# Kernel tuning notes

Measured on AMD Instinct MI355X. Metric: run time of the kernel, lower is better.

Reference implementation:

```python
import jax, jax.numpy as jnp
from jax import lax
import numpy as np
import math

B, T, HID = 4, 2048, 1024
NH, KS, INTER = 8, 4, 2816
HD = HID // NH
CHUNK = 32
EPS = 1e-6


def setup_inputs() -> dict:
    key = jax.random.key(0)
    ks = jax.random.split(key, 16)
    def w(k, shape, fan_in):
        return jax.random.normal(k, shape, jnp.float32) * (1.0 / math.sqrt(fan_in))
    logit = math.log(0.95 / 0.05)
    return {
        'x': jax.random.normal(ks[0], (B, T, HID), jnp.float32),
        'qkv_w': w(ks[1], (3 * HID, HID), HID),
        'out_proj_w': w(ks[2], (HID, HID), HID),
        'out_gate_w': w(ks[3], (HID, HID), HID),
        'out_gate_b': jnp.zeros((HID,), jnp.float32),
        'decay_param': jnp.full((NH,), logit, jnp.float32),
        'conv_w': w(ks[4], (HID, 1, KS), KS),      # depthwise: [out, in/groups=1, k]
        'conv_b': jnp.zeros((HID,), jnp.float32),
        'pw_w': w(ks[5], (HID, HID), HID),
        'gate_w': w(ks[6], (HID, 2 * HID), 2 * HID),
        'w1': w(ks[7], (INTER, HID), HID),
        'w2': w(ks[8], (INTER, HID), HID),
        'w3': w(ks[9], (HID, INTER), INTER),
        'norm1_w': jnp.ones((HID,), jnp.float32),
        'norm2_w': jnp.ones((HID,), jnp.float32),
    }


def rmsnorm(x, w, eps=EPS):
    ms = jnp.mean(jnp.square(x), axis=-1, keepdims=True)
    return x * lax.rsqrt(ms + eps) * w


def decay_scan(x, decay, init):
    # inclusive scan out[t] = decay*out[t-1] + x[t]; x:[B,NH,T,HD], decay:[1,NH,1], init:[B,NH,HD]
    b, h, t, d = x.shape
    c = min(CHUNK, t)
    log_d = jnp.log(jnp.maximum(decay.astype(jnp.float32), 1e-8))        # [1,NH,1]
    idx = jnp.arange(c, dtype=jnp.float32)
    log_p = log_d[..., None] * idx[None, None, :, None]                  # [1,NH,c,1]
    p, inv_p = jnp.exp(log_p), jnp.exp(-log_p)
    init_p = jnp.exp(log_d[..., None] * (idx + 1.0)[None, None, :, None])
    xc = x.astype(jnp.float32).reshape(b, h, t // c, c, d)
    xc = jnp.moveaxis(xc, 2, 0)                                          # [Nc,B,NH,c,HD]
    def step(state, chunk):
        cs = jnp.cumsum(chunk * inv_p, axis=2)
        out = cs * p + state[:, :, None, :] * init_p
        return out[:, :, -1, :], out
    _, outs = lax.scan(step, init.astype(jnp.float32), xc)
    out = jnp.moveaxis(outs, 0, 2).reshape(b, h, t, d)
    return out.astype(x.dtype)


def _forward(x, qkv_w, out_proj_w, out_gate_w, out_gate_b, decay_param,
             conv_w, conv_b, pw_w, gate_w, w1, w2, w3, norm1_w, norm2_w):
    b, t, _ = x.shape
    h = rmsnorm(x, norm1_w)

    # ---- LocalConv (depthwise causal conv + pointwise) ----
    xc = jnp.transpose(h, (0, 2, 1))                                     # [B,HID,T]
    pad = jnp.zeros((b, HID, KS - 1), x.dtype)
    xc = jnp.concatenate([pad, xc], axis=2)
    conv = lax.conv_general_dilated(xc, conv_w, (1,), 'VALID',
                                    dimension_numbers=('NCH', 'OIH', 'NCH'),
                                    feature_group_count=HID)
    conv = conv + conv_b[None, :, None]
    conv = jnp.transpose(conv, (0, 2, 1))                                # [B,T,HID]
    local = jnp.einsum('bth,oh->bto', jax.nn.silu(conv), pw_w)

    # ---- LinearAttention ----
    qkv = jnp.einsum('bth,oh->bto', h, qkv_w)
    q, k, v = jnp.split(qkv, 3, axis=-1)
    def heads(z):
        return jnp.transpose(z.reshape(b, t, NH, HD), (0, 2, 1, 3))      # [B,NH,T,HD]
    q, k, v = heads(q), heads(k), heads(v)
    q = jax.nn.elu(q) + 1.0
    k = jax.nn.elu(k) + 1.0
    decay = jax.nn.sigmoid(decay_param).reshape(1, NH, 1)
    zero_state = jnp.zeros((b, NH, HD), x.dtype)
    running_kv = decay_scan(k * v, decay, zero_state)
    running_ks = decay_scan(k, decay, zero_state)
    den = jnp.maximum(jnp.sum(q * running_ks, axis=-1, keepdims=True), 1e-6)
    o = q * running_kv / den                                             # [B,NH,T,HD]
    v_direct = jnp.transpose(v, (0, 2, 1, 3)).reshape(b, t, HID)
    o = jnp.transpose(o, (0, 2, 1, 3)).reshape(b, t, HID)
    g = jax.nn.sigmoid(jnp.einsum('bth,oh->bto', o, out_gate_w) + out_gate_b)
    o = g * o + (1.0 - g) * v_direct
    attn = jnp.einsum('bth,oh->bto', o, out_proj_w)

    # ---- Gate fusion of local/global, residual ----
    comb = jnp.concatenate([local, attn], axis=-1)
    gmix = jax.nn.sigmoid(jnp.einsum('bth,oh->bto', comb, gate_w))
    x = x + gmix * local + (1.0 - gmix) * attn

    # ---- FFN (SwiGLU) + residual ----
    h2 = rmsnorm(x, norm2_w)
    ffn = jnp.einsum('bti,oi->bto',
                     jax.nn.silu(jnp.einsum('bth,ih->bti', h2, w1)) *
                     jnp.einsum('bth,ih->bti', h2, w2), w3)
    return x + ffn


def reference(x, qkv_w, out_proj_w, out_gate_w, out_gate_b, decay_param,
              conv_w, conv_b, pw_w, gate_w, w1, w2, w3, norm1_w, norm2_w):
    return _forward(x, qkv_w, out_proj_w, out_gate_w, out_gate_b, decay_param,
                    conv_w, conv_b, pw_w, gate_w, w1, w2, w3, norm1_w, norm2_w)
```

## Files before the change

### kernel.cpp

```cpp
#include <hip/hip_runtime.h>
#include <math.h>

static constexpr int Bc    = 4;
static constexpr int Tc    = 2048;
static constexpr int HIDc  = 1024;
static constexpr int NHc   = 8;
static constexpr int HDc   = 128;
static constexpr int Mrows = Bc * Tc;
static constexpr int INTERc= 2816;
static constexpr int CH    = 64;
static constexpr int NC    = Tc / CH;

typedef _Float16 f16;
typedef __attribute__((ext_vector_type(8))) _Float16 f16x8;
typedef __attribute__((ext_vector_type(4))) float f32x4;
typedef unsigned short u16;

union H8 { f16 h[8]; int4 v; u16 u[8]; };
union H4 { f16 h[4]; int2 v; u16 u[4]; };
union F4 { float4 v; float a[4]; };

static __device__ __forceinline__ float sigm(float x) { return 1.0f / (1.0f + expf(-x)); }
static __device__ __forceinline__ float silu(float x) { return x * sigm(x); }
static __device__ __forceinline__ float elu1(float x) { return x > 0.0f ? x + 1.0f : expf(x); }

static __device__ __forceinline__ float h2f(u16 u){ f16 h; __builtin_memcpy(&h,&u,2); return (float)h; }
static __device__ __forceinline__ u16 f2h(float x){ f16 h=(f16)x; u16 u; __builtin_memcpy(&u,&h,2); return u; }
static __device__ __forceinline__ float rec2(u16 h, u16 l){ return h2f(h) + h2f(l); }
static __device__ __forceinline__ void fsplit(float v, u16& h, u16& l){ h = f2h(v); l = f2h(v - h2f(h)); }

static __device__ __forceinline__ void gld16(const u16* g, u16* l)
{
    __builtin_amdgcn_global_load_lds((const __attribute__((address_space(1))) void*)g,
                                     (__attribute__((address_space(3))) void*)l,
                                     16, 0, 0);
}

__global__ __launch_bounds__(256) void wcvt_k(const float* __restrict__ src,
                                              u16* __restrict__ dst, int n8)
{
    const int i = blockIdx.x * 256 + threadIdx.x;
    if (i >= n8) return;
    F4 a, b; a.v = ((const float4*)src)[i * 2]; b.v = ((const float4*)src)[i * 2 + 1];
    H8 o;
    #pragma unroll
    for (int u = 0; u < 4; u++) { o.h[u] = (f16)a.a[u]; o.h[4 + u] = (f16)b.a[u]; }
    ((int4*)dst)[i] = o.v;
}

template<int INPAIR>
__global__ __launch_bounds__(256) void rmsnorm_k(const float* __restrict__ xf,
                                                 const u16* __restrict__ xhi,
                                                 const u16* __restrict__ xlo,
                                                 const float* __restrict__ w,
                                                 u16* __restrict__ ohi,
                                                 u16* __restrict__ olo)
{
    const int row = blockIdx.x;
    const int tid = threadIdx.x;
    const size_t off = (size_t)row * HIDc + tid * 4;
    float xv[4];
    if constexpr (INPAIR) {
        H4 H, L;
        H.v = *(const int2*)(xhi + off);
        L.v = *(const int2*)(xlo + off);
        #pragma unroll
        for (int u = 0; u < 4; u++) xv[u] = (float)H.h[u] + (float)L.h[u];
    } else {
        F4 f; f.v = *(const float4*)(xf + off);
        #pragma unroll
        for (int u = 0; u < 4; u++) xv[u] = f.a[u];
    }
    float ss = xv[0]*xv[0] + xv[1]*xv[1] + xv[2]*xv[2] + xv[3]*xv[3];
    #pragma unroll
    for (int o = 32; o > 0; o >>= 1) ss += __shfl_xor(ss, o);
    __shared__ float sred[4];
    if ((tid & 63) == 0) sred[tid >> 6] = ss;
    __syncthreads();
    const float tot = sred[0] + sred[1] + sred[2] + sred[3];
    const float scale = rsqrtf(tot * (1.0f / (float)HIDc) + 1e-6f);
    F4 wv; wv.v = *(const float4*)(w + tid * 4);
    H4 OH, OL;
    #pragma unroll
    for (int u = 0; u < 4; u++) {
        u16 hh, ll; fsplit(xv[u] * scale * wv.a[u], hh, ll);
        OH.u[u] = hh; OL.u[u] = ll;
    }
    *(int2*)(ohi + off) = OH.v;
    *(int2*)(olo + off) = OL.v;
}

__global__ __launch_bounds__(256) void conv_k(const u16* __restrict__ hhi,
                                              const u16* __restrict__ hlo,
                                              const float* __restrict__ cw,
                                              const float* __restrict__ cb,
                                              u16* __restrict__ ohi,
                                              u16* __restrict__ olo)
{
    const int row = blockIdx.x;
    const int t   = row & (Tc - 1);
    const int ch4 = threadIdx.x * 4;
    const float* wp = cw + (size_t)ch4 * 4;
    F4 bias; bias.v = *(const float4*)(cb + ch4);
    F4 acc;
    #pragma unroll
    for (int u = 0; u < 4; u++) acc.a[u] = bias.a[u];
    #pragma unroll
    for (int j = 0; j < 4; j++) {
        const int tt = t - 3 + j;
        if (tt >= 0) {
            const size_t off = ((size_t)row + j - 3) * HIDc + ch4;
            H4 H, L;
            H.v = *(const int2*)(hhi + off);
            L.v = *(const int2*)(hlo + off);
            #pragma unroll
            for (int u = 0; u < 4; u++) acc.a[u] += ((float)H.h[u] + (float)L.h[u]) * wp[u * 4 + j];
        }
    }
    H4 OH, OL;
    #pragma unroll
    for (int u = 0; u < 4; u++) {
        u16 hh, ll; fsplit(silu(acc.a[u]), hh, ll);
        OH.u[u] = hh; OL.u[u] = ll;
    }
    const size_t off = (size_t)row * HIDc + ch4;
    *(int2*)(ohi + off) = OH.v;
    *(int2*)(olo + off) = OL.v;
}

__global__ __launch_bounds__(64) void scan1_k(u16* __restrict__ khi, u16* __restrict__ klo,
                                              const u16* __restrict__ vhi, const u16* __restrict__ vlo,
                                              u16* __restrict__ shi, u16* __restrict__ slo,
                                              const float* __restrict__ dp)
{
    const int bid = blockIdx.x;
    const int c   = bid & (NC - 1);
    const int bh  = bid >> 5;
    const int b   = bh >> 3, hh = bh & 7;
    const int lane = threadIdx.x;
    const float dec = sigm(dp[hh]);
    const size_t base = (size_t)b * Tc * HIDc + (size_t)(c * CH) * HIDc + hh * HDc + lane * 2;
    float skv0 = 0.f, skv1 = 0.f, sks0 = 0.f, sks1 = 0.f;
    for (int t = 0; t < CH; t++) {
        const size_t p = base + (size_t)t * HIDc;
        const unsigned kh = *(const unsigned*)(khi + p);
        const unsigned kl = *(const unsigned*)(klo + p);
        const unsigned vh = *(const unsigned*)(vhi + p);
        const unsigned vl = *(const unsigned*)(vlo + p);
        const float kx = elu1(rec2((u16)kh, (u16)kl));
        const float ky = elu1(rec2((u16)(kh >> 16), (u16)(kl >> 16)));
        const float vx = rec2((u16)vh, (u16)vl);
        const float vy = rec2((u16)(vh >> 16), (u16)(vl >> 16));
        skv0 = dec * skv0 + kx * vx;
        skv1 = dec * skv1 + ky * vy;
        sks0 = dec * sks0 + kx;
        sks1 = dec * sks1 + ky;
        u16 h0, l0, h1, l1;
        fsplit(skv0, h0, l0); fsplit(skv1, h1, l1);
        *(unsigned*)(khi + p) = (unsigned)h0 | ((unsigned)h1 << 16);
        *(unsigned*)(klo + p) = (unsigned)l0 | ((unsigned)l1 << 16);
        fsplit(sks0, h0, l0); fsplit(sks1, h1, l1);
        *(unsigned*)(shi + p) = (unsigned)h0 | ((unsigned)h1 << 16);
        *(unsigned*)(slo + p) = (unsigned)l0 | ((unsigned)l1 << 16);
    }
}

__global__ __launch_bounds__(64) void scan2_k(u16* __restrict__ qhi, u16* __restrict__ qlo,
                                              const u16* __restrict__ skvhi, const u16* __restrict__ skvlo,
                                              const u16* __restrict__ skshi, const u16* __restrict__ skslo,
                                              const float* __restrict__ dp)
{
    const int bid = blockIdx.x;
    const int c   = bid & (NC - 1);
    const int bh  = bid >> 5;
    const int b   = bh >> 3, hh = bh & 7;
    const int lane = threadIdx.x;
    const float dec = sigm(dp[hh]);
    float dCH = dec;
    #pragma unroll
    for (int i = 0; i < 6; i++) dCH *= dCH;
    const size_t rowbase = (size_t)b * Tc * HIDc + hh * HDc + lane * 2;

    float ckv0 = 0.f, ckv1 = 0.f, cks0 = 0.f, cks1 = 0.f;
    for (int j = 0; j < c; j++) {
        const size_t p = rowbase + (size_t)(j * CH + CH - 1) * HIDc;
        const unsigned ah = *(const unsigned*)(skvhi + p);
        const unsigned al = *(const unsigned*)(skvlo + p);
        const unsigned bh2 = *(const unsigned*)(skshi + p);
        const unsigned bl2 = *(const unsigned*)(skslo + p);
        ckv0 = ckv0 * dCH + rec2((u16)ah, (u16)al);
        ckv1 = ckv1 * dCH + rec2((u16)(ah >> 16), (u16)(al >> 16));
        cks0 = cks0 * dCH + rec2((u16)bh2, (u16)bl2);
        cks1 = cks1 * dCH + rec2((u16)(bh2 >> 16), (u16)(bl2 >> 16));
    }

    const size_t cbase = rowbase + (size_t)(c * CH) * HIDc;
    float pw = dec;
    for (int t = 0; t < CH; t++) {
        const size_t p = cbase + (size_t)t * HIDc;
        const unsigned qh = *(const unsigned*)(qhi + p);
        const unsigned ql = *(const unsigned*)(qlo + p);
        const unsigned ah = *(const unsigned*)(skvhi + p);
        const unsigned al = *(const unsigned*)(skvlo + p);
        const unsigned bh2 = *(const unsigned*)(skshi + p);
        const unsigned bl2 = *(const unsigned*)(skslo + p);
        const float qx = elu1(rec2((u16)qh, (u16)ql));
        const float qy = elu1(rec2((u16)(qh >> 16), (u16)(ql >> 16)));
        const float skv0 = rec2((u16)ah, (u16)al) + pw * ckv0;
        const float skv1 = rec2((u16)(ah >> 16), (u16)(al >> 16)) + pw * ckv1;
        const float sks0 = rec2((u16)bh2, (u16)bl2) + pw * cks0;
        const float sks1 = rec2((u16)(bh2 >> 16), (u16)(bl2 >> 16)) + pw * cks1;
        float part = qx * sks0 + qy * sks1;
        #pragma unroll
        for (int o = 32; o > 0; o >>= 1) part += __shfl_xor(part, o);
        const float inv = 1.0f / fmaxf(part, 1e-6f);
        u16 h0, l0, h1, l1;
        fsplit(qx * skv0 * inv, h0, l0);
        fsplit(qy * skv1 * inv, h1, l1);
        *(unsigned*)(qhi + p) = (unsigned)h0 | ((unsigned)h1 << 16);
        *(unsigned*)(qlo + p) = (unsigned)l0 | ((unsigned)l1 << 16);
        pw *= dec;
    }
}

template<int MODE, int PRE>
__global__ __launch_bounds__(256) void gemm_f16_k(
    const u16* __restrict__ Ahi, const u16* __restrict__ Alo,
    const u16* __restrict__ A2hi, const u16* __restrict__ A2lo, int lda,
    const u16* __restrict__ Wh, const float* __restrict__ Wf,
    float* __restrict__ Cout,
    u16* __restrict__ Chi, u16* __restrict__ Clo, int ldc,
    int K, int kSplit, int nx,
    const float* __restrict__ bias,
    const float* __restrict__ E0f,
    const u16* __restrict__ E0hi, const u16* __restrict__ E0lo, int ldE0,
    const u16* __restrict__ E1hi, const u16* __restrict__ E1lo, int ldE1,
    const u16* __restrict__ E2hi, const u16* __restrict__ E2lo, int ldE2)
{
    __shared__ __align__(16) u16 Ah[4][128][8];
    __shared__ __align__(16) u16 Al[4][128][8];
    __shared__ __align__(16) u16 Bs[4][128][8];

    const int tid  = threadIdx.x;
    const int lane = tid & 63;
    const int wv   = tid >> 6;
    const int wr   = wv >> 1, wc = wv & 1;
    const int lr   = lane & 15, lk = lane >> 4;

    const int cpx = gridDim.x >> 3;
    int bid = blockIdx.x;
    bid = (bid & 7) * cpx + (bid >> 3);
    const int n0 = (bid % nx) * 128;
    const int m0 = (bid / nx) * 128;

    f32x4 acc[4][4];
    #pragma unroll
    for (int i = 0; i < 4; i++)
        #pragma unroll
        for (int j = 0; j < 4; j++)
            acc[i][j] = (f32x4){0.f, 0.f, 0.f, 0.f};

    for (int k0 = 0; k0 < K; k0 += 32) {
        const u16* ah = Ahi; const u16* al = Alo; int kb = k0;
        if constexpr (MODE == 4) {
            if (k0 >= kSplit) { ah = A2hi; al = A2lo; kb = k0 - kSplit; }
        }
        const size_t a0off = (size_t)(m0 + lane) * lda + kb + wv * 8;
        const size_t a1off = a0off + (size_t)64 * lda;
        F4 wreg[4];
        size_t w0off = 0, w1off = 0;
        if constexpr (PRE) {
            w0off = (size_t)(n0 + lane) * K + k0 + wv * 8;
            w1off = w0off + (size_t)64 * K;
        } else {
            const float* wp0 = Wf + (size_t)(n0 + lane) * K + k0 + wv * 8;
            const float* wp1 = wp0 + (size_t)64 * K;
            wreg[0].v = *(const float4*)(wp0);
            wreg[1].v = *(const float4*)(wp0 + 4);
            wreg[2].v = *(const float4*)(wp1);
            wreg[3].v = *(const float4*)(wp1 + 4);
        }
        __syncthreads();
        gld16(ah + a0off, &Ah[wv][0][0]);
        gld16(ah + a1off, &Ah[wv][64][0]);
        gld16(al + a0off, &Al[wv][0][0]);
        gld16(al + a1off, &Al[wv][64][0]);
        if constexpr (PRE) {
            gld16(Wh + w0off, &Bs[wv][0][0]);
            gld16(Wh + w1off, &Bs[wv][64][0]);
        } else {
            H8 W0, W1;
            #pragma unroll
            for (int e = 0; e < 8; e++) {
                W0.h[e] = (f16)wreg[e >> 2].a[e & 3];
                W1.h[e] = (f16)wreg[2 + (e >> 2)].a[e & 3];
            }
            *(int4*)&Bs[wv][lane][0]      = W0.v;
            *(int4*)&Bs[wv][64 + lane][0] = W1.v;
        }
        __syncthreads();
        f16x8 av[4], au[4], bv[4];
        #pragma unroll
        for (int fi = 0; fi < 4; fi++) {
            av[fi] = *(const f16x8*)&Ah[lk][wr * 64 + fi * 16 + lr][0];
            au[fi] = *(const f16x8*)&Al[lk][wr * 64 + fi * 16 + lr][0];
            bv[fi] = *(const f16x8*)&Bs[lk][wc * 64 + fi * 16 + lr][0];
        }
        #pragma unroll
        for (int i = 0; i < 4; i++)
            #pragma unroll
            for (int j = 0; j < 4; j++) {
                acc[i][j] = __builtin_amdgcn_mfma_f32_16x16x32_f16(av[i], bv[j], acc[i][j], 0, 0, 0);
                acc[i][j] = __builtin_amdgcn_mfma_f32_16x16x32_f16(au[i], bv[j], acc[i][j], 0, 0, 0);
            }
    }

    #pragma unroll
    for (int i = 0; i < 4; i++) {
        #pragma unroll
        for (int j = 0; j < 4; j++) {
            #pragma unroll
            for (int v = 0; v < 4; v++) {
                const size_t r = (size_t)(m0 + wr * 64 + i * 16 + lk * 4 + v);
                const int c = n0 + wc * 64 + j * 16 + lr;
                const size_t idx = r * (size_t)ldc + c;
                float val = acc[i][j][v];
                if constexpr (MODE == 1) {
                    val = silu(val);
                } else if constexpr (MODE == 2) {
                    val = rec2(Chi[idx], Clo[idx]) * val;
                } else if constexpr (MODE == 3) {
                    const float g = sigm(val + bias[c]);
                    const size_t i0 = r * (size_t)ldE0 + c, i1 = r * (size_t)ldE1 + c;
                    val = g * rec2(E0hi[i0], E0lo[i0]) + (1.0f - g) * rec2(E1hi[i1], E1lo[i1]);
                } else if constexpr (MODE == 4) {
                    const float g = sigm(val);
                    const size_t i1 = r * (size_t)ldE1 + c, i2 = r * (size_t)ldE2 + c;
                    val = E0f[r * (size_t)ldE0 + c] + g * rec2(E1hi[i1], E1lo[i1])
                          + (1.0f - g) * rec2(E2hi[i2], E2lo[i2]);
                } else if constexpr (MODE == 6) {
                    Cout[idx] = rec2(Chi[idx], Clo[idx]) + val;
                    continue;
                }
                u16 hh, ll; fsplit(val, hh, ll);
                Chi[idx] = hh; Clo[idx] = ll;
            }
        }
    }
}

template<int MODE>
static inline void launch_gemm(bool pre, int nblocks, int nx, hipStream_t stream,
    const u16* Ahi, const u16* Alo, const u16* A2hi, const u16* A2lo, int lda,
    const u16* Wh, const float* Wf,
    float* Cout, u16* Chi, u16* Clo, int ldc, int K, int kSplit,
    const float* bias, const float* E0f,
    const u16* E0hi, const u16* E0lo, int ldE0,
    const u16* E1hi, const u16* E1lo, int ldE1,
    const u16* E2hi, const u16* E2lo, int ldE2)
{
    if (pre)
        gemm_f16_k<MODE, 1><<<dim3(nblocks), dim3(256), 0, stream>>>(Ahi, Alo, A2hi, A2lo, lda, Wh, Wf,
            Cout, Chi, Clo, ldc, K, kSplit, nx, bias, E0f, E0hi, E0lo, ldE0, E1hi, E1lo, ldE1, E2hi, E2lo, ldE2);
    else
        gemm_f16_k<MODE, 0><<<dim3(nblocks), dim3(256), 0, stream>>>(Ahi, Alo, A2hi, A2lo, lda, Wh, Wf,
            Cout, Chi, Clo, ldc, K, kSplit, nx, bias, E0f, E0hi, E0lo, ldE0, E1hi, E1lo, ldE1, E2hi, E2lo, ldE2);
}

extern "C" void kernel_launch(void* const* d_in, const int* in_sizes, int n_in,
                              void* d_out, int out_size, void* d_ws, size_t ws_size,
                              hipStream_t stream)
{
    const float* x           = (const float*)d_in[0];
    const float* qkv_w       = (const float*)d_in[1];
    const float* out_proj_w  = (const float*)d_in[2];
    const float* out_gate_w  = (const float*)d_in[3];
    const float* out_gate_b  = (const float*)d_in[4];
    const float* decay_param = (const float*)d_in[5];
    const float* conv_w      = (const float*)d_in[6];
    const float* conv_b      = (const float*)d_in[7];
    const float* pw_w        = (const float*)d_in[8];
    const float* gate_w      = (const float*)d_in[9];
    const float* w1          = (const float*)d_in[10];
    const float* w2          = (const float*)d_in[11];
    const float* w3          = (const float*)d_in[12];
    const float* norm1_w     = (const float*)d_in[13];
    const float* norm2_w     = (const float*)d_in[14];
    float* OUT = (float*)d_out;

    float* ws = (float*)d_ws;
    const size_t S8 = (size_t)Mrows * HIDc;
    u16* P0h = (u16*)(ws + 0 * S8); u16* P0l = P0h + S8;
    u16* P1h = (u16*)(ws + 1 * S8); u16* P1l = P1h + S8;
    u16* P2h = (u16*)(ws + 2 * S8); u16* P2l = P2h + S8;
    u16* P3h = (u16*)(ws + 3 * S8); u16* P3l = P3h + S8;
    u16* OUTh = (u16*)OUT;          u16* OUTl = OUTh + S8;
    u16* T1h = P1h;                 u16* T1l = P1h + (size_t)Mrows * INTERc;

    constexpr size_t SZ_QKV  = (size_t)3 * HIDc * HIDc;
    constexpr size_t SZ_SQ   = (size_t)HIDc * HIDc;
    constexpr size_t SZ_GATE = (size_t)2 * HIDc * HIDc;
    constexpr size_t SZ_W1   = (size_t)INTERc * HIDc;
    constexpr size_t W_ELEMS = SZ_QKV + 3 * SZ_SQ + SZ_GATE + 3 * SZ_W1;
    const bool pre = (ws_size >= 4 * S8 * sizeof(float) + W_ELEMS * sizeof(u16));

    u16* wb   = (u16*)(ws + 4 * S8);
    u16* qkvH = wb;
    u16* pwH  = qkvH + SZ_QKV;
    u16* ogH  = pwH  + SZ_SQ;
    u16* opH  = ogH  + SZ_SQ;
    u16* gaH  = opH  + SZ_SQ;
    u16* w1H  = gaH  + SZ_GATE;
    u16* w2H  = w1H  + SZ_W1;
    u16* w3H  = w2H  + SZ_W1;

    const dim3 blk(256);
    const int nb8  = 8 * (Mrows / 128);
    const int nb22 = 22 * (Mrows / 128);
    const u16* nu = nullptr;

    if (pre) {
        wcvt_k<<<(int)(SZ_QKV / 8 / 256), blk, 0, stream>>>(qkv_w, qkvH, (int)(SZ_QKV / 8));
        wcvt_k<<<(int)(SZ_SQ  / 8 / 256), blk, 0, stream>>>(pw_w,  pwH,  (int)(SZ_SQ  / 8));
        wcvt_k<<<(int)(SZ_SQ  / 8 / 256), blk, 0, stream>>>(out_gate_w, ogH, (int)(SZ_SQ / 8));
        wcvt_k<<<(int)(SZ_SQ  / 8 / 256), blk, 0, stream>>>(out_proj_w, opH, (int)(SZ_SQ / 8));
        wcvt_k<<<(int)(SZ_GATE/ 8 / 256), blk, 0, stream>>>(gate_w, gaH, (int)(SZ_GATE / 8));
        wcvt_k<<<(int)(SZ_W1  / 8 / 256), blk, 0, stream>>>(w1, w1H, (int)(SZ_W1 / 8));
        wcvt_k<<<(int)(SZ_W1  / 8 / 256), blk, 0, stream>>>(w2, w2H, (int)(SZ_W1 / 8));
        wcvt_k<<<(int)(SZ_W1  / 8 / 256), blk, 0, stream>>>(w3, w3H, (int)(SZ_W1 / 8));
    }

    rmsnorm_k<0><<<Mrows, blk, 0, stream>>>(x, nullptr, nullptr, norm1_w, P0h, P0l);
    conv_k<<<Mrows, blk, 0, stream>>>(P0h, P0l, conv_w, conv_b, P1h, P1l);
    launch_gemm<0>(pre, nb8, 8, stream, P1h, P1l, nu, nu, HIDc, pwH, pw_w,
                   nullptr, P2h, P2l, HIDc, HIDc, 0, nullptr, nullptr,
                   nu, nu, 0, nu, nu, 0, nu, nu, 0);
    launch_gemm<0>(pre, nb8, 8, stream, P0h, P0l, nu, nu, HIDc, qkvH, qkv_w,
                   nullptr, P1h, P1l, HIDc, HIDc, 0, nullptr, nullptr,
                   nu, nu, 0, nu, nu, 0, nu, nu, 0);
    launch_gemm<0>(pre, nb8, 8, stream, P0h, P0l, nu, nu, HIDc, qkvH + SZ_SQ, qkv_w + SZ_SQ,
                   nullptr, P3h, P3l, HIDc, HIDc, 0, nullptr, nullptr,
                   nu, nu, 0, nu, nu, 0, nu, nu, 0);
    launch_gemm<0>(pre, nb8, 8, stream, P0h, P0l, nu, nu, HIDc, qkvH + 2 * SZ_SQ, qkv_w + 2 * SZ_SQ,
                   nullptr, OUTh, OUTl, HIDc, HIDc, 0, nullptr, nullptr,
                   nu, nu, 0, nu, nu, 0, nu, nu, 0);
    scan1_k<<<Bc * NHc * NC, dim3(64), 0, stream>>>(P3h, P3l, OUTh, OUTl, P0h, P0l, decay_param);
    scan2_k<<<Bc * NHc * NC, dim3(64), 0, stream>>>(P1h, P1l, P3h, P3l, P0h, P0l, decay_param);
    launch_gemm<3>(pre, nb8, 8, stream, P1h, P1l, nu, nu, HIDc, ogH, out_gate_w,
                   nullptr, P0h, P0l, HIDc, HIDc, 0, out_gate_b, nullptr,
                   P1h, P1l, HIDc, OUTh, OUTl, HIDc, nu, nu, 0);
    launch_gemm<0>(pre, nb8, 8, stream, P0h, P0l, nu, nu, HIDc, opH, out_proj_w,
                   nullptr, P3h, P3l, HIDc, HIDc, 0, nullptr, nullptr,
                   nu, nu, 0, nu, nu, 0, nu, nu, 0);
    launch_gemm<4>(pre, nb8, 8, stream, P2h, P2l, P3h, P3l, HIDc, gaH, gate_w,
                   nullptr, P0h, P0l, HIDc, 2 * HIDc, HIDc, nullptr, x,
                   nu, nu, HIDc, P2h, P2l, HIDc, P3h, P3l, HIDc);
    rmsnorm_k<1><<<Mrows, blk, 0, stream>>>(nullptr, P0h, P0l, norm2_w, OUTh, OUTl);
    launch_gemm<1>(pre, nb22, 22, stream, OUTh, OUTl, nu, nu, HIDc, w1H, w1,
                   nullptr, T1h, T1l, INTERc, HIDc, 0, nullptr, nullptr,
                   nu, nu, 0, nu, nu, 0, nu, nu, 0);
    launch_gemm<2>(pre, nb22, 22, stream, OUTh, OUTl, nu, nu, HIDc, w2H, w2,
                   nullptr, T1h, T1l, INTERc, HIDc, 0, nullptr, nullptr,
                   nu, nu, 0, nu, nu, 0, nu, nu, 0);
    launch_gemm<6>(pre, nb8, 8, stream, T1h, T1l, nu, nu, INTERc, w3H, w3,
                   OUT, P0h, P0l, HIDc, INTERc, 0, nullptr, nullptr,
                   nu, nu, 0, nu, nu, 0, nu, nu, 0);
}
```

Baseline: 1.285 ms.

## Fuse QKV projections and SwiGLU up-projections, double GEMM K-step

Raises the GEMM K-step from 32 to 64 with larger shared tiles, halving barrier count per tile. Merges the three QKV projections into one launch (mode 5) that routes each output column plane to its own buffer. Adds a dual-B kernel computing silu(A·W1)·(A·W2) in one pass, so the activation tiles are read once and the intermediate T1 round-trip is avoided. The changes raise LDS use and register pressure (two accumulator sets in the dual kernel), which can lower occupancy.

```diff
diff --git a/kernel.cpp b/kernel.cpp
--- a/kernel.cpp
+++ b/kernel.cpp
@@ -237,9 +237,9 @@
     const u16* __restrict__ E1hi, const u16* __restrict__ E1lo, int ldE1,
     const u16* __restrict__ E2hi, const u16* __restrict__ E2lo, int ldE2)
 {
-    __shared__ __align__(16) u16 Ah[4][128][8];
-    __shared__ __align__(16) u16 Al[4][128][8];
-    __shared__ __align__(16) u16 Bs[4][128][8];
+    __shared__ __align__(16) u16 Ah[8][128][8];
+    __shared__ __align__(16) u16 Al[8][128][8];
+    __shared__ __align__(16) u16 Bs[8][128][8];
 
     const int tid  = threadIdx.x;
     const int lane = tid & 63;
@@ -260,61 +260,76 @@
         for (int j = 0; j < 4; j++)
             acc[i][j] = (f32x4){0.f, 0.f, 0.f, 0.f};
 
-    for (int k0 = 0; k0 < K; k0 += 32) {
+    for (int k0 = 0; k0 < K; k0 += 64) {
         const u16* ah = Ahi; const u16* al = Alo; int kb = k0;
         if constexpr (MODE == 4) {
             if (k0 >= kSplit) { ah = A2hi; al = A2lo; kb = k0 - kSplit; }
         }
-        const size_t a0off = (size_t)(m0 + lane) * lda + kb + wv * 8;
-        const size_t a1off = a0off + (size_t)64 * lda;
-        F4 wreg[4];
-        size_t w0off = 0, w1off = 0;
-        if constexpr (PRE) {
-            w0off = (size_t)(n0 + lane) * K + k0 + wv * 8;
-            w1off = w0off + (size_t)64 * K;
-        } else {
-            const float* wp0 = Wf + (size_t)(n0 + lane) * K + k0 + wv * 8;
-            const float* wp1 = wp0 + (size_t)64 * K;
-            wreg[0].v = *(const float4*)(wp0);
-            wreg[1].v = *(const float4*)(wp0 + 4);
-            wreg[2].v = *(const float4*)(wp1);
-            wreg[3].v = *(const float4*)(wp1 + 4);
+        F4 wreg[8];
+        if constexpr (!PRE) {
+            #pragma unroll
+            for (int q = 0; q < 2; q++) {
+                const float* wp0 = Wf + (size_t)(n0 + lane) * K + k0 + (2 * wv + q) * 8;
+                const float* wp1 = wp0 + (size_t)64 * K;
+                wreg[q * 4 + 0].v = *(const float4*)(wp0);
+                wreg[q * 4 + 1].v = *(const float4*)(wp0 + 4);
+                wreg[q * 4 + 2].v = *(const float4*)(wp1);
+                wreg[q * 4 + 3].v = *(const float4*)(wp1 + 4);
+            }
         }
         __syncthreads();
-        gld16(ah + a0off, &Ah[wv][0][0]);
-        gld16(ah + a1off, &Ah[wv][64][0]);
-        gld16(al + a0off, &Al[wv][0][0]);
-        gld16(al + a1off, &Al[wv][64][0]);
-        if constexpr (PRE) {
-            gld16(Wh + w0off, &Bs[wv][0][0]);
-            gld16(Wh + w1off, &Bs[wv][64][0]);
-        } else {
-            H8 W0, W1;
-            #pragma unroll
-            for (int e = 0; e < 8; e++) {
-                W0.h[e] = (f16)wreg[e >> 2].a[e & 3];
-                W1.h[e] = (f16)wreg[2 + (e >> 2)].a[e & 3];
+        #pragma unroll
+        for (int q = 0; q < 2; q++) {
+            const int cc = 2 * wv + q;
+            const size_t a0 = (size_t)(m0 + lane) * lda + kb + cc * 8;
+            gld16(ah + a0, &Ah[cc][0][0]);
+            gld16(ah + a0 + (size_t)64 * lda, &Ah[cc][64][0]);
+            gld16(al + a0, &Al[cc][0][0]);
+            gld16(al + a0 + (size_t)64 * lda, &Al[cc][64][0]);
+            if constexpr (PRE) {
+                const size_t w0 = (size_t)(n0 + lane) * K + k0 + cc * 8;
+                gld16(Wh + w0, &Bs[cc][0][0]);
+                gld16(Wh + w0 + (size_t)64 * K, &Bs[cc][64][0]);
+            } else {
+                H8 W0, W1;
+                #pragma unroll
+                for (int e = 0; e < 8; e++) {
+                    W0.h[e] = (f16)wreg[q * 4 + (e >> 2)].a[e & 3];
+                    W1.h[e] = (f16)wreg[q * 4 + 2 + (e >> 2)].a[e & 3];
+                }
+                *(int4*)&Bs[cc][lane][0]      = W0.v;
+                *(int4*)&Bs[cc][64 + lane][0] = W1.v;
             }
-            *(int4*)&Bs[wv][lane][0]      = W0.v;
-            *(int4*)&Bs[wv][64 + lane][0] = W1.v;
         }
         __syncthreads();
-        f16x8 av[4], au[4], bv[4];
-        #pragma unroll
-        for (int fi = 0; fi < 4; fi++) {
-            av[fi] = *(const f16x8*)&Ah[lk][wr * 64 + fi * 16 + lr][0];
-            au[fi] = *(const f16x8*)&Al[lk][wr * 64 + fi * 16 + lr][0];
-            bv[fi] = *(const f16x8*)&Bs[lk][wc * 64 + fi * 16 + lr][0];
-        }
-        #pragma unroll
-        for (int i = 0; i < 4; i++)
-            #pragma unroll
-            for (int j = 0; j < 4; j++) {
-                acc[i][j] = __builtin_amdgcn_mfma_f32_16x16x32_f16(av[i], bv[j], acc[i][j], 0, 0, 0);
-                acc[i][j] = __builtin_amdgcn_mfma_f32_16x16x32_f16(au[i], bv[j], acc[i][j], 0, 0, 0);
+        #pragma unroll
+        for (int ks = 0; ks < 2; ks++) {
+            const int ck = ks * 4 + lk;
+            f16x8 av[4], au[4], bv[4];
+            #pragma unroll
+            for (int fi = 0; fi < 4; fi++) {
+                av[fi] = *(const f16x8*)&Ah[ck][wr * 64 + fi * 16 + lr][0];
+                au[fi] = *(const f16x8*)&Al[ck][wr * 64 + fi * 16 + lr][0];
+                bv[fi] = *(const f16x8*)&Bs[ck][wc * 64 + fi * 16 + lr][0];
             }
-    }
-
+            #pragma unroll
+            for (int i = 0; i < 4; i++)
+                #pragma unroll
+                for (int j = 0; j < 4; j++) {
+                    acc[i][j] = __builtin_amdgcn_mfma_f32_16x16x32_f16(av[i], bv[j], acc[i][j], 0, 0, 0);
+                    acc[i][j] = __builtin_amdgcn_mfma_f32_16x16x32_f16(au[i], bv[j], acc[i][j], 0, 0, 0);
+                }
+        }
+    }
+
+    u16* dsth = Chi; u16* dstl = Clo;
+    int nbase = n0;
+    if constexpr (MODE == 5) {
+        const int plane = n0 >> 10;
+        nbase = n0 & 1023;
+        if (plane == 1)      { dsth = const_cast<u16*>(E0hi); dstl = const_cast<u16*>(E0lo); }
+        else if (plane == 2) { dsth = const_cast<u16*>(E1hi); dstl = const_cast<u16*>(E1lo); }
+    }
     #pragma unroll
     for (int i = 0; i < 4; i++) {
         #pragma unroll
@@ -322,7 +337,7 @@
             #pragma unroll
             for (int v = 0; v < 4; v++) {
                 const size_t r = (size_t)(m0 + wr * 64 + i * 16 + lk * 4 + v);
-                const int c = n0 + wc * 64 + j * 16 + lr;
+                const int c = nbase + wc * 64 + j * 16 + lr;
                 const size_t idx = r * (size_t)ldc + c;
                 float val = acc[i][j][v];
                 if constexpr (MODE == 1) {
@@ -343,6 +358,95 @@
                     continue;
                 }
                 u16 hh, ll; fsplit(val, hh, ll);
+                dsth[idx] = hh; dstl[idx] = ll;
+            }
+        }
+    }
+}
+
+__global__ __launch_bounds__(256) void gemm_dual_k(
+    const u16* __restrict__ Ahi, const u16* __restrict__ Alo, int lda,
+    const u16* __restrict__ W1h, const u16* __restrict__ W2h,
+    u16* __restrict__ Chi, u16* __restrict__ Clo, int ldc,
+    int K, int nx)
+{
+    __shared__ __align__(16) u16 Ah[8][128][8];
+    __shared__ __align__(16) u16 Al[8][128][8];
+    __shared__ __align__(16) u16 B1[8][128][8];
+    __shared__ __align__(16) u16 B2[8][128][8];
+
+    const int tid  = threadIdx.x;
+    const int lane = tid & 63;
+    const int wv   = tid >> 6;
+    const int wr   = wv >> 1, wc = wv & 1;
+    const int lr   = lane & 15, lk = lane >> 4;
+
+    const int cpx = gridDim.x >> 3;
+    int bid = blockIdx.x;
+    bid = (bid & 7) * cpx + (bid >> 3);
+    const int n0 = (bid % nx) * 128;
+    const int m0 = (bid / nx) * 128;
+
+    f32x4 acc1[4][4], acc2[4][4];
+    #pragma unroll
+    for (int i = 0; i < 4; i++)
+        #pragma unroll
+        for (int j = 0; j < 4; j++) {
+            acc1[i][j] = (f32x4){0.f, 0.f, 0.f, 0.f};
+            acc2[i][j] = (f32x4){0.f, 0.f, 0.f, 0.f};
+        }
+
+    for (int k0 = 0; k0 < K; k0 += 64) {
+        __syncthreads();
+        #pragma unroll
+        for (int q = 0; q < 2; q++) {
+            const int cc = 2 * wv + q;
+            const size_t a0 = (size_t)(m0 + lane) * lda + k0 + cc * 8;
+            gld16(Ahi + a0, &Ah[cc][0][0]);
+            gld16(Ahi + a0 + (size_t)64 * lda, &Ah[cc][64][0]);
+            gld16(Alo + a0, &Al[cc][0][0]);
+            gld16(Alo + a0 + (size_t)64 * lda, &Al[cc][64][0]);
+            const size_t w0 = (size_t)(n0 + lane) * K + k0 + cc * 8;
+            gld16(W1h + w0, &B1[cc][0][0]);
+            gld16(W1h + w0 + (size_t)64 * K, &B1[cc][64][0]);
+            gld16(W2h + w0, &B2[cc][0][0]);
+            gld16(W2h + w0 + (size_t)64 * K, &B2[cc][64][0]);
+        }
+        __syncthreads();
+        #pragma unroll
+        for (int ks = 0; ks < 2; ks++) {
+            const int ck = ks * 4 + lk;
+            f16x8 av[4], au[4], b1[4], b2[4];
+            #pragma unroll
+            for (int fi = 0; fi < 4; fi++) {
+                av[fi] = *(const f16x8*)&Ah[ck][wr * 64 + fi * 16 + lr][0];
+                au[fi] = *(const f16x8*)&Al[ck][wr * 64 + fi * 16 + lr][0];
+                b1[fi] = *(const f16x8*)&B1[ck][wc * 64 + fi * 16 + lr][0];
+                b2[fi] = *(const f16x8*)&B2[ck][wc * 64 + fi * 16 + lr][0];
+            }
+            #pragma unroll
+            for (int i = 0; i < 4; i++)
+                #pragma unroll
+                for (int j = 0; j < 4; j++) {
+                    acc1[i][j] = __builtin_amdgcn_mfma_f32_16x16x32_f16(av[i], b1[j], acc1[i][j], 0, 0, 0);
+                    acc1[i][j] = __builtin_amdgcn_mfma_f32_16x16x32_f16(au[i], b1[j], acc1[i][j], 0, 0, 0);
+                    acc2[i][j] = __builtin_amdgcn_mfma_f32_16x16x32_f16(av[i], b2[j], acc2[i][j], 0, 0, 0);
+                    acc2[i][j] = __builtin_amdgcn_mfma_f32_16x16x32_f16(au[i], b2[j], acc2[i][j], 0, 0, 0);
+                }
+        }
+    }
+
+    #pragma unroll
+    for (int i = 0; i < 4; i++) {
+        #pragma unroll
+        for (int j = 0; j < 4; j++) {
+            #pragma unroll
+            for (int v = 0; v < 4; v++) {
+                const size_t r = (size_t)(m0 + wr * 64 + i * 16 + lk * 4 + v);
+                const int c = n0 + wc * 64 + j * 16 + lr;
+                const size_t idx = r * (size_t)ldc + c;
+                const float val = silu(acc1[i][j][v]) * acc2[i][j][v];
+                u16 hh, ll; fsplit(val, hh, ll);
                 Chi[idx] = hh; Clo[idx] = ll;
             }
         }
@@ -417,6 +521,7 @@
     const dim3 blk(256);
     const int nb8  = 8 * (Mrows / 128);
     const int nb22 = 22 * (Mrows / 128);
+    const int nb24 = 24 * (Mrows / 128);
     const u16* nu = nullptr;
 
     if (pre) {
@@ -435,15 +540,21 @@
     launch_gemm<0>(pre, nb8, 8, stream, P1h, P1l, nu, nu, HIDc, pwH, pw_w,
                    nullptr, P2h, P2l, HIDc, HIDc, 0, nullptr, nullptr,
                    nu, nu, 0, nu, nu, 0, nu, nu, 0);
-    launch_gemm<0>(pre, nb8, 8, stream, P0h, P0l, nu, nu, HIDc, qkvH, qkv_w,
-                   nullptr, P1h, P1l, HIDc, HIDc, 0, nullptr, nullptr,
-                   nu, nu, 0, nu, nu, 0, nu, nu, 0);
-    launch_gemm<0>(pre, nb8, 8, stream, P0h, P0l, nu, nu, HIDc, qkvH + SZ_SQ, qkv_w + SZ_SQ,
-                   nullptr, P3h, P3l, HIDc, HIDc, 0, nullptr, nullptr,
-                   nu, nu, 0, nu, nu, 0, nu, nu, 0);
-    launch_gemm<0>(pre, nb8, 8, stream, P0h, P0l, nu, nu, HIDc, qkvH + 2 * SZ_SQ, qkv_w + 2 * SZ_SQ,
-                   nullptr, OUTh, OUTl, HIDc, HIDc, 0, nullptr, nullptr,
-                   nu, nu, 0, nu, nu, 0, nu, nu, 0);
+    if (pre) {
+        launch_gemm<5>(pre, nb24, 24, stream, P0h, P0l, nu, nu, HIDc, qkvH, qkv_w,
+                       nullptr, P1h, P1l, HIDc, HIDc, 0, nullptr, nullptr,
+                       P3h, P3l, HIDc, OUTh, OUTl, HIDc, nu, nu, 0);
+    } else {
+        launch_gemm<0>(pre, nb8, 8, stream, P0h, P0l, nu, nu, HIDc, qkvH, qkv_w,
+                       nullptr, P1h, P1l, HIDc, HIDc, 0, nullptr, nullptr,
+                       nu, nu, 0, nu, nu, 0, nu, nu, 0);
+        launch_gemm<0>(pre, nb8, 8, stream, P0h, P0l, nu, nu, HIDc, qkvH + SZ_SQ, qkv_w + SZ_SQ,
+                       nullptr, P3h, P3l, HIDc, HIDc, 0, nullptr, nullptr,
+                       nu, nu, 0, nu, nu, 0, nu, nu, 0);
+        launch_gemm<0>(pre, nb8, 8, stream, P0h, P0l, nu, nu, HIDc, qkvH + 2 * SZ_SQ, qkv_w + 2 * SZ_SQ,
+                       nullptr, OUTh, OUTl, HIDc, HIDc, 0, nullptr, nullptr,
+                       nu, nu, 0, nu, nu, 0, nu, nu, 0);
+    }
     scan1_k<<<Bc * NHc * NC, dim3(64), 0, stream>>>(P3h, P3l, OUTh, OUTl, P0h, P0l, decay_param);
     scan2_k<<<Bc * NHc * NC, dim3(64), 0, stream>>>(P1h, P1l, P3h, P3l, P0h, P0l, decay_param);
     launch_gemm<3>(pre, nb8, 8, stream, P1h, P1l, nu, nu, HIDc, ogH, out_gate_w,
@@ -456,12 +567,17 @@
                    nullptr, P0h, P0l, HIDc, 2 * HIDc, HIDc, nullptr, x,
                    nu, nu, HIDc, P2h, P2l, HIDc, P3h, P3l, HIDc);
     rmsnorm_k<1><<<Mrows, blk, 0, stream>>>(nullptr, P0h, P0l, norm2_w, OUTh, OUTl);
-    launch_gemm<1>(pre, nb22, 22, stream, OUTh, OUTl, nu, nu, HIDc, w1H, w1,
-                   nullptr, T1h, T1l, INTERc, HIDc, 0, nullptr, nullptr,
-                   nu, nu, 0, nu, nu, 0, nu, nu, 0);
-    launch_gemm<2>(pre, nb22, 22, stream, OUTh, OUTl, nu, nu, HIDc, w2H, w2,
-                   nullptr, T1h, T1l, INTERc, HIDc, 0, nullptr, nullptr,
-                   nu, nu, 0, nu, nu, 0, nu, nu, 0);
+    if (pre) {
+        gemm_dual_k<<<dim3(nb22), blk, 0, stream>>>(OUTh, OUTl, HIDc, w1H, w2H,
+                                                    T1h, T1l, INTERc, HIDc, 22);
+    } else {
+        launch_gemm<1>(pre, nb22, 22, stream, OUTh, OUTl, nu, nu, HIDc, w1H, w1,
+                       nullptr, T1h, T1l, INTERc, HIDc, 0, nullptr, nullptr,
+                       nu, nu, 0, nu, nu, 0, nu, nu, 0);
+        launch_gemm<2>(pre, nb22, 22, stream, OUTh, OUTl, nu, nu, HIDc, w2H, w2,
+                       nullptr, T1h, T1l, INTERc, HIDc, 0, nullptr, nullptr,
+                       nu, nu, 0, nu, nu, 0, nu, nu, 0);
+    }
     launch_gemm<6>(pre, nb8, 8, stream, T1h, T1l, nu, nu, INTERc, w3H, w3,
                    OUT, P0h, P0l, HIDc, INTERc, 0, nullptr, nullptr,
                    nu, nu, 0, nu, nu, 0, nu, nu, 0);
```

After: 1.324 ms. 1.03x slower.

## Double-buffer GEMM shared-memory tiles and fuse QKV projections into one launch

Applied to the files above, without the earlier changes.

The GEMM main loop now uses two shared-memory buffers. Global loads for the next K-tile are issued before the MFMAs on the current tile, which removes one of the two barriers per iteration. This is meant to overlap memory latency with compute, at the cost of doubling LDS per block, which may lower occupancy. A new MODE 5 writes the three QKV projection outputs into separate planes, selected by the column block, so the three 1024-wide GEMMs run as a single 3072-wide launch when pre-converted weights are available.

```diff
diff --git a/kernel.cpp b/kernel.cpp
--- a/kernel.cpp
+++ b/kernel.cpp
@@ -237,9 +237,9 @@
     const u16* __restrict__ E1hi, const u16* __restrict__ E1lo, int ldE1,
     const u16* __restrict__ E2hi, const u16* __restrict__ E2lo, int ldE2)
 {
-    __shared__ __align__(16) u16 Ah[4][128][8];
-    __shared__ __align__(16) u16 Al[4][128][8];
-    __shared__ __align__(16) u16 Bs[4][128][8];
+    __shared__ __align__(16) u16 Ah[2][4][128][8];
+    __shared__ __align__(16) u16 Al[2][4][128][8];
+    __shared__ __align__(16) u16 Bs[2][4][128][8];
 
     const int tid  = threadIdx.x;
     const int lane = tid & 63;
@@ -260,51 +260,52 @@
         for (int j = 0; j < 4; j++)
             acc[i][j] = (f32x4){0.f, 0.f, 0.f, 0.f};
 
-    for (int k0 = 0; k0 < K; k0 += 32) {
+    auto stage = [&](int t, int b) {
+        const int k0 = t * 32;
         const u16* ah = Ahi; const u16* al = Alo; int kb = k0;
         if constexpr (MODE == 4) {
             if (k0 >= kSplit) { ah = A2hi; al = A2lo; kb = k0 - kSplit; }
         }
-        const size_t a0off = (size_t)(m0 + lane) * lda + kb + wv * 8;
-        const size_t a1off = a0off + (size_t)64 * lda;
-        F4 wreg[4];
-        size_t w0off = 0, w1off = 0;
+        const size_t a0 = (size_t)(m0 + lane) * lda + kb + wv * 8;
+        gld16(ah + a0, &Ah[b][wv][0][0]);
+        gld16(ah + a0 + (size_t)64 * lda, &Ah[b][wv][64][0]);
+        gld16(al + a0, &Al[b][wv][0][0]);
+        gld16(al + a0 + (size_t)64 * lda, &Al[b][wv][64][0]);
         if constexpr (PRE) {
-            w0off = (size_t)(n0 + lane) * K + k0 + wv * 8;
-            w1off = w0off + (size_t)64 * K;
+            const size_t w0 = (size_t)(n0 + lane) * K + k0 + wv * 8;
+            gld16(Wh + w0, &Bs[b][wv][0][0]);
+            gld16(Wh + w0 + (size_t)64 * K, &Bs[b][wv][64][0]);
         } else {
             const float* wp0 = Wf + (size_t)(n0 + lane) * K + k0 + wv * 8;
             const float* wp1 = wp0 + (size_t)64 * K;
-            wreg[0].v = *(const float4*)(wp0);
-            wreg[1].v = *(const float4*)(wp0 + 4);
-            wreg[2].v = *(const float4*)(wp1);
-            wreg[3].v = *(const float4*)(wp1 + 4);
-        }
-        __syncthreads();
-        gld16(ah + a0off, &Ah[wv][0][0]);
-        gld16(ah + a1off, &Ah[wv][64][0]);
-        gld16(al + a0off, &Al[wv][0][0]);
-        gld16(al + a1off, &Al[wv][64][0]);
-        if constexpr (PRE) {
-            gld16(Wh + w0off, &Bs[wv][0][0]);
-            gld16(Wh + w1off, &Bs[wv][64][0]);
-        } else {
+            F4 g0, g1, g2, g3;
+            g0.v = *(const float4*)(wp0); g1.v = *(const float4*)(wp0 + 4);
+            g2.v = *(const float4*)(wp1); g3.v = *(const float4*)(wp1 + 4);
             H8 W0, W1;
             #pragma unroll
-            for (int e = 0; e < 8; e++) {
-                W0.h[e] = (f16)wreg[e >> 2].a[e & 3];
-                W1.h[e] = (f16)wreg[2 + (e >> 2)].a[e & 3];
+            for (int e = 0; e < 4; e++) {
+                W0.h[e] = (f16)g0.a[e]; W0.h[4 + e] = (f16)g1.a[e];
+                W1.h[e] = (f16)g2.a[e]; W1.h[4 + e] = (f16)g3.a[e];
             }
-            *(int4*)&Bs[wv][lane][0]      = W0.v;
-            *(int4*)&Bs[wv][64 + lane][0] = W1.v;
+            *(int4*)&Bs[b][wv][lane][0]      = W0.v;
+            *(int4*)&Bs[b][wv][64 + lane][0] = W1.v;
         }
-        __syncthreads();
+    };
+
+    const int NT = K / 32;
+    stage(0, 0);
+    __syncthreads();
+
+    for (int t = 0; ; ) {
+        const int cur = t & 1;
+        const bool more = (t + 1 < NT);
+        if (more) stage(t + 1, cur ^ 1);
         f16x8 av[4], au[4], bv[4];
         #pragma unroll
         for (int fi = 0; fi < 4; fi++) {
-            av[fi] = *(const f16x8*)&Ah[lk][wr * 64 + fi * 16 + lr][0];
-            au[fi] = *(const f16x8*)&Al[lk][wr * 64 + fi * 16 + lr][0];
-            bv[fi] = *(const f16x8*)&Bs[lk][wc * 64 + fi * 16 + lr][0];
+            av[fi] = *(const f16x8*)&Ah[cur][lk][wr * 64 + fi * 16 + lr][0];
+            au[fi] = *(const f16x8*)&Al[cur][lk][wr * 64 + fi * 16 + lr][0];
+            bv[fi] = *(const f16x8*)&Bs[cur][lk][wc * 64 + fi * 16 + lr][0];
         }
         #pragma unroll
         for (int i = 0; i < 4; i++)
@@ -313,8 +314,19 @@
                 acc[i][j] = __builtin_amdgcn_mfma_f32_16x16x32_f16(av[i], bv[j], acc[i][j], 0, 0, 0);
                 acc[i][j] = __builtin_amdgcn_mfma_f32_16x16x32_f16(au[i], bv[j], acc[i][j], 0, 0, 0);
             }
-    }
-
+        if (!more) break;
+        __syncthreads();
+        ++t;
+    }
+
+    u16* dsth = Chi; u16* dstl = Clo;
+    int nbase = n0;
+    if constexpr (MODE == 5) {
+        const int plane = n0 >> 10;
+        nbase = n0 & 1023;
+        if (plane == 1)      { dsth = const_cast<u16*>(E0hi); dstl = const_cast<u16*>(E0lo); }
+        else if (plane == 2) { dsth = const_cast<u16*>(E1hi); dstl = const_cast<u16*>(E1lo); }
+    }
     #pragma unroll
     for (int i = 0; i < 4; i++) {
         #pragma unroll
@@ -322,7 +334,7 @@
             #pragma unroll
             for (int v = 0; v < 4; v++) {
                 const size_t r = (size_t)(m0 + wr * 64 + i * 16 + lk * 4 + v);
-                const int c = n0 + wc * 64 + j * 16 + lr;
+                const int c = nbase + wc * 64 + j * 16 + lr;
                 const size_t idx = r * (size_t)ldc + c;
                 float val = acc[i][j][v];
                 if constexpr (MODE == 1) {
@@ -343,7 +355,7 @@
                     continue;
                 }
                 u16 hh, ll; fsplit(val, hh, ll);
-                Chi[idx] = hh; Clo[idx] = ll;
+                dsth[idx] = hh; dstl[idx] = ll;
             }
         }
     }
@@ -417,6 +429,7 @@
     const dim3 blk(256);
     const int nb8  = 8 * (Mrows / 128);
     const int nb22 = 22 * (Mrows / 128);
+    const int nb24 = 24 * (Mrows / 128);
     const u16* nu = nullptr;
 
     if (pre) {
@@ -435,15 +448,21 @@
     launch_gemm<0>(pre, nb8, 8, stream, P1h, P1l, nu, nu, HIDc, pwH, pw_w,
                    nullptr, P2h, P2l, HIDc, HIDc, 0, nullptr, nullptr,
                    nu, nu, 0, nu, nu, 0, nu, nu, 0);
-    launch_gemm<0>(pre, nb8, 8, stream, P0h, P0l, nu, nu, HIDc, qkvH, qkv_w,
-                   nullptr, P1h, P1l, HIDc, HIDc, 0, nullptr, nullptr,
-                   nu, nu, 0, nu, nu, 0, nu, nu, 0);
-    launch_gemm<0>(pre, nb8, 8, stream, P0h, P0l, nu, nu, HIDc, qkvH + SZ_SQ, qkv_w + SZ_SQ,
-                   nullptr, P3h, P3l, HIDc, HIDc, 0, nullptr, nullptr,
-                   nu, nu, 0, nu, nu, 0, nu, nu, 0);
-    launch_gemm<0>(pre, nb8, 8, stream, P0h, P0l, nu, nu, HIDc, qkvH + 2 * SZ_SQ, qkv_w + 2 * SZ_SQ,
-                   nullptr, OUTh, OUTl, HIDc, HIDc, 0, nullptr, nullptr,
-                   nu, nu, 0, nu, nu, 0, nu, nu, 0);
+    if (pre) {
+        launch_gemm<5>(pre, nb24, 24, stream, P0h, P0l, nu, nu, HIDc, qkvH, qkv_w,
+                       nullptr, P1h, P1l, HIDc, HIDc, 0, nullptr, nullptr,
+                       P3h, P3l, HIDc, OUTh, OUTl, HIDc, nu, nu, 0);
+    } else {
+        launch_gemm<0>(pre, nb8, 8, stream, P0h, P0l, nu, nu, HIDc, qkvH, qkv_w,
+                       nullptr, P1h, P1l, HIDc, HIDc, 0, nullptr, nullptr,
+                       nu, nu, 0, nu, nu, 0, nu, nu, 0);
+        launch_gemm<0>(pre, nb8, 8, stream, P0h, P0l, nu, nu, HIDc, qkvH + SZ_SQ, qkv_w + SZ_SQ,
+                       nullptr, P3h, P3l, HIDc, HIDc, 0, nullptr, nullptr,
+                       nu, nu, 0, nu, nu, 0, nu, nu, 0);
+        launch_gemm<0>(pre, nb8, 8, stream, P0h, P0l, nu, nu, HIDc, qkvH + 2 * SZ_SQ, qkv_w + 2 * SZ_SQ,
+                       nullptr, OUTh, OUTl, HIDc, HIDc, 0, nullptr, nullptr,
+                       nu, nu, 0, nu, nu, 0, nu, nu, 0);
+    }
     scan1_k<<<Bc * NHc * NC, dim3(64), 0, stream>>>(P3h, P3l, OUTh, OUTl, P0h, P0l, decay_param);
     scan2_k<<<Bc * NHc * NC, dim3(64), 0, stream>>>(P1h, P1l, P3h, P3l, P0h, P0l, decay_param);
     launch_gemm<3>(pre, nb8, 8, stream, P1h, P1l, nu, nu, HIDc, ogH, out_gate_w,
```

New measurement: 1.341 ms. +4.4%, slower.
